# Kernel optimization log

Hardware: AMD Instinct MI355X
Metric: run time of the kernel (lower is better)

The kernel has to match this reference:

```python
import jax, jax.numpy as jnp
import numpy as np

N = 100000      # nodes
E = 1600000     # edges (avg degree 16)
F_IN = 128      # node feature dim
F_OUT = 128     # GCN output dim


def setup_inputs() -> dict:
    key = jax.random.key(0)
    ks = jax.random.split(key, 11)
    s = 0.05  # weight scale to keep activations sane
    return {
        "x": jax.random.normal(ks[0], (N, F_IN), jnp.float32),
        "edge_index": jax.random.randint(ks[1], (2, E), 0, N, jnp.int32),
        "W": jax.random.normal(ks[2], (F_IN, F_OUT), jnp.float32) * s,
        "p": jax.random.normal(ks[3], (F_IN,), jnp.float32),
        "w_ih": jax.random.normal(ks[4], (3 * F_OUT, F_IN), jnp.float32) * s,
        "w_hh": jax.random.normal(ks[5], (3 * F_OUT, F_OUT), jnp.float32) * s,
        "b_ih": jax.random.normal(ks[6], (3 * F_OUT,), jnp.float32) * s,
        "b_hh": jax.random.normal(ks[7], (3 * F_OUT,), jnp.float32) * s,
        "conv_bias": jax.random.normal(ks[8], (F_OUT,), jnp.float32) * s,
        "lin_w": jax.random.normal(ks[9], (1, F_OUT), jnp.float32) * s,
        "lin_b": jax.random.normal(ks[10], (1,), jnp.float32) * s,
    }


def reference(x, edge_index, W, p, w_ih, w_hh, b_ih, b_hh, conv_bias, lin_w, lin_b):
    n_nodes = x.shape[0]
    k, H = W.shape  # k = F_IN rows, H = F_OUT hidden size

    # --- TopK summarize: pick k nodes, gate by tanh(score) -> X_tilde [k, F_IN]
    scores = x @ p / jnp.linalg.norm(p)
    top_vals, top_idx = jax.lax.top_k(scores, k)
    x_tilde = x[top_idx] * jnp.tanh(top_vals)[:, None]

    # --- one GRU step evolving W (hidden state = rows of W)
    gi = x_tilde @ w_ih.T + b_ih   # [k, 3H]
    gh = W @ w_hh.T + b_hh         # [k, 3H]
    r = jax.nn.sigmoid(gi[:, :H] + gh[:, :H])
    z = jax.nn.sigmoid(gi[:, H:2 * H] + gh[:, H:2 * H])
    n = jnp.tanh(gi[:, 2 * H:] + r * gh[:, 2 * H:])
    W_new = (1.0 - z) * n + z * W  # [F_IN, F_OUT]

    # --- GCN conv with fixed W: sym-normalized adjacency with self loops
    row, col = edge_index[0], edge_index[1]
    deg = jax.ops.segment_sum(jnp.ones_like(row, dtype=x.dtype), col,
                              num_segments=n_nodes) + 1.0  # +1 for self loop
    dinv = jax.lax.rsqrt(deg)
    xw = x @ W_new                                   # [N, F_OUT]
    coef = dinv[row] * dinv[col]                     # [E]
    agg = jax.ops.segment_sum(xw[row] * coef[:, None], col, num_segments=n_nodes)
    agg = agg + xw * (dinv * dinv)[:, None] + conv_bias  # self-loop term + bias

    # --- head: ReLU + Linear(F_OUT, 1)
    h = jax.nn.relu(agg)
    return h @ lin_w.T + lin_b  # [N, 1]
```

## Files before the change

kernel.cpp:

```cpp
#include <hip/hip_runtime.h>
#include <math.h>

#define N_NODES 100000
#define N_EDGES 1600000
#define F 128

#define BSH 9
#define NBUCK 196
#define BCAP 10240
#define PB_EDGES 4096

typedef unsigned int u32;
typedef unsigned short u16;
typedef __attribute__((ext_vector_type(8))) short short8;
typedef __attribute__((ext_vector_type(4))) float floatx4;


__device__ __forceinline__ u32 key_of(float s) {
    u32 u = __float_as_uint(s);
    return (u & 0x80000000u) ? ~u : (u | 0x80000000u);
}

__device__ __forceinline__ float wave_reduce(float v) {
    #pragma unroll
    for (int off = 32; off > 0; off >>= 1) v += __shfl_down(v, off, 64);
    return v;
}

__device__ __forceinline__ u16 f2bf(float f) {
    u32 u = __float_as_uint(f);
    u += 0x7fffu + ((u >> 16) & 1u);
    return (u16)(u >> 16);
}

__device__ __forceinline__ float bflo(u32 b) { return __uint_as_float(b << 16); }
__device__ __forceinline__ float bfhi(u32 b) { return __uint_as_float(b & 0xffff0000u); }


__global__ void k_scores(const float* __restrict__ x, const float* __restrict__ p,
                         float* __restrict__ scores, u32* __restrict__ hist16) {
    int node = blockIdx.x * 4 + (threadIdx.x >> 6);
    int lane = threadIdx.x & 63;
    if (node >= N_NODES) return;
    float2 xv = *(const float2*)&x[(size_t)node * F + lane * 2];
    float2 pv = *(const float2*)&p[lane * 2];
    float d = xv.x * pv.x + xv.y * pv.y;
    d = wave_reduce(d);
    if (lane == 0) {
        scores[node] = d;
        atomicAdd(&hist16[key_of(d) >> 16], 1u);
    }
}


__global__ __launch_bounds__(1024) void k_scan16(const u32* __restrict__ hist16,
                                                 u32* __restrict__ state) {
    __shared__ u32 a[1024];
    int t = threadIdx.x;
    const uint4* h4 = (const uint4*)hist16;
    u32 local = 0;
    #pragma unroll
    for (int i = 0; i < 16; i++) {
        uint4 v = h4[t * 16 + i];
        local += v.x + v.y + v.z + v.w;
    }
    a[t] = local;
    __syncthreads();
    for (int off = 1; off < 1024; off <<= 1) {
        u32 add = (t + off < 1024) ? a[t + off] : 0u;
        __syncthreads();
        a[t] += add;
        __syncthreads();
    }
    u32 S_above = (t == 1023) ? 0u : a[t + 1];
    if (S_above < 128u && a[t] >= 128u) {
        u32 cum = S_above;
        for (int v = t * 64 + 63; v >= t * 64; v--) {
            cum += hist16[v];
            if (cum >= 128u) { state[0] = (u32)v; break; }
        }
    }
}

__global__ void k_collect16(const float* __restrict__ scores, u32* __restrict__ state,
                            u32* __restrict__ cand) {
    u32 T = state[0] << 16;
    int i = blockIdx.x * blockDim.x + threadIdx.x;
    if (i < N_NODES) {
        if (key_of(scores[i]) >= T) {
            u32 pos = atomicAdd(&state[2], 1u);
            if (pos < 2048u) cand[pos] = (u32)i;
        }
    }
}

__global__ void k_assemble16(const float* __restrict__ scores, const float* __restrict__ p,
                             const u32* __restrict__ state, const u32* __restrict__ cand,
                             u32* __restrict__ top_idx, float* __restrict__ gate) {
    __shared__ u32 ci[2048];
    __shared__ float csc[2048];
    __shared__ float s_inv;
    int t = threadIdx.x;
    if (t < 64) {
        float2 pv = *(const float2*)&p[t * 2];
        float d = pv.x * pv.x + pv.y * pv.y;
        d = wave_reduce(d);
        if (t == 0) s_inv = rsqrtf(d);
    }
    u32 nc = state[2]; if (nc > 2048u) nc = 2048u;
    for (u32 i = t; i < nc; i += 256) { u32 ix = cand[i]; ci[i] = ix; csc[i] = scores[ix]; }
    __syncthreads();
    for (u32 i = t; i < nc; i += 256) {
        u32 myk = key_of(csc[i]);
        u32 myi = ci[i];
        int rank = 0;
        for (u32 j = 0; j < nc; j++) {
            u32 ok = key_of(csc[j]);
            rank += (int)((ok > myk) || (ok == myk && ci[j] < myi));
        }
        if (rank < 128) {
            top_idx[rank] = myi;
            gate[rank] = tanhf(csc[i] * s_inv);
        }
    }
}


__global__ __launch_bounds__(256) void k_ggemm(const float* __restrict__ x,
                                               const float* __restrict__ W,
                                               const float* __restrict__ w_ih,
                                               const float* __restrict__ w_hh,
                                               const u32* __restrict__ top_idx,
                                               const float* __restrict__ gate,
                                               float* __restrict__ G) {
    __shared__ float As[32][128];
    __shared__ float Bs[64][131];
    int t = threadIdx.x;
    int k0 = blockIdx.x * 32;
    int by = blockIdx.y;
    int j0 = by * 64;
    bool is_gi = (by < 6);
    #pragma unroll
    for (int i = 0; i < 4; i++) {
        int l = t + i * 256;
        int row = l >> 5, c4 = l & 31;
        float4 v;
        if (is_gi) {
            u32 idx = top_idx[k0 + row];
            float gt = gate[k0 + row];
            v = *(const float4*)&x[(size_t)idx * F + c4 * 4];
            v.x *= gt; v.y *= gt; v.z *= gt; v.w *= gt;
        } else {
            v = *(const float4*)&W[(k0 + row) * F + c4 * 4];
        }
        *(float4*)&As[row][c4 * 4] = v;
    }
    const float* mat = is_gi ? w_ih : w_hh;
    int jbase = is_gi ? j0 : (j0 - 384);
    #pragma unroll
    for (int i = 0; i < 8; i++) {
        int l = t + i * 256;
        int row = l >> 5, c4 = l & 31;
        float4 v = *(const float4*)&mat[(jbase + row) * F + c4 * 4];
        Bs[row][c4 * 4 + 0] = v.x; Bs[row][c4 * 4 + 1] = v.y;
        Bs[row][c4 * 4 + 2] = v.z; Bs[row][c4 * 4 + 3] = v.w;
    }
    __syncthreads();
    int ty = t >> 5, tx = t & 31;
    float acc[4][2] = {};
    #pragma unroll 4
    for (int f = 0; f < 128; f++) {
        float b0 = Bs[tx * 2][f], b1 = Bs[tx * 2 + 1][f];
        #pragma unroll
        for (int i = 0; i < 4; i++) {
            float a = As[ty * 4 + i][f];
            acc[i][0] += a * b0;
            acc[i][1] += a * b1;
        }
    }
    #pragma unroll
    for (int i = 0; i < 4; i++) {
        int k = k0 + ty * 4 + i;
        G[(size_t)k * 768 + j0 + tx * 2 + 0] = acc[i][0];
        G[(size_t)k * 768 + j0 + tx * 2 + 1] = acc[i][1];
    }
}


__global__ void k_gate(const float* __restrict__ G, const float* __restrict__ W,
                       const float* __restrict__ b_ih, const float* __restrict__ b_hh,
                       float* __restrict__ Wnew, u16* __restrict__ Bfrag) {
    int idx = blockIdx.x * blockDim.x + threadIdx.x;
    int k = idx >> 7, h = idx & 127;
    const float* gk = &G[(size_t)k * 768];
    float gir = gk[h]       + b_ih[h];
    float giz = gk[128 + h] + b_ih[128 + h];
    float gin = gk[256 + h] + b_ih[256 + h];
    float ghr = gk[384 + h] + b_hh[h];
    float ghz = gk[512 + h] + b_hh[128 + h];
    float ghn = gk[640 + h] + b_hh[256 + h];
    float wv  = W[k * F + h];
    float rg = 1.0f / (1.0f + expf(-(gir + ghr)));
    float z  = 1.0f / (1.0f + expf(-(giz + ghz)));
    float n  = tanhf(gin + rg * ghn);
    float val = (1.0f - z) * n + z * wv;
    Wnew[k * F + h] = val;
    int nb = h >> 4, kc = k >> 5, q = (k >> 3) & 3, m = h & 15, jj = k & 7;
    Bfrag[(((nb * 4 + kc) * 64) + q * 16 + m) * 8 + jj] = f2bf(val);
}


__global__ void k_part(const int* __restrict__ ei, u32* __restrict__ gcur,
                       u32* __restrict__ pairs) {
    __shared__ u32 lh[NBUCK];
    __shared__ u32 lbase[NBUCK];
    int t = threadIdx.x;
    int e0 = blockIdx.x * PB_EDGES;
    int e1 = e0 + PB_EDGES; if (e1 > N_EDGES) e1 = N_EDGES;
    for (int i = t; i < NBUCK; i += 256) lh[i] = 0u;
    __syncthreads();
    for (int e = e0 + t; e < e1; e += 256)
        atomicAdd(&lh[((u32)ei[N_EDGES + e]) >> BSH], 1u);
    __syncthreads();
    for (int b = t; b < NBUCK; b += 256) {
        u32 c = lh[b];
        lbase[b] = c ? atomicAdd(&gcur[b], c) : 0u;
        lh[b] = 0u;
    }
    __syncthreads();
    for (int e = e0 + t; e < e1; e += 256) {
        u32 d = (u32)ei[N_EDGES + e];
        u32 b = d >> BSH;
        u32 pos = lbase[b] + atomicAdd(&lh[b], 1u);
        pairs[(size_t)b * BCAP + pos] = ((d & 511u) << 17) | (u32)ei[e];
    }
}

__global__ __launch_bounds__(256) void k_csr(const u32* __restrict__ pairs,
                                             const u32* __restrict__ gcur,
                                             u32* __restrict__ offs,
                                             float* __restrict__ dinv,
                                             u32* __restrict__ ebuf) {
    __shared__ u32 h[512];
    __shared__ u32 sc[512];
    __shared__ u32 ps[256];
    int b = blockIdx.x, t = threadIdx.x;
    u32 pv = (t < NBUCK) ? gcur[t] : 0u;
    ps[t] = pv;
    __syncthreads();
    for (int off = 1; off < 256; off <<= 1) {
        u32 add = (t >= off) ? ps[t - off] : 0u;
        __syncthreads();
        ps[t] += add;
        __syncthreads();
    }
    u32 base = ps[b] - gcur[b];
    u32 cnt  = gcur[b];
    const u32* seg = pairs + (size_t)b * BCAP;
    u32 lo = (u32)b << BSH;
    for (int i = t; i < 512; i += 256) h[i] = 0u;
    __syncthreads();
    for (u32 i = t; i < cnt; i += 256)
        atomicAdd(&h[seg[i] >> 17], 1u);
    __syncthreads();
    for (int i = t; i < 512; i += 256) sc[i] = h[i];
    __syncthreads();
    for (int off = 1; off < 512; off <<= 1) {
        int i0 = t, i1 = t + 256;
        u32 v0 = (i0 >= off) ? sc[i0 - off] : 0u;
        u32 v1 = (i1 >= off) ? sc[i1 - off] : 0u;
        __syncthreads();
        sc[i0] += v0; sc[i1] += v1;
        __syncthreads();
    }
    int nn = N_NODES - (int)lo; if (nn > 512) nn = 512;
    for (int i = t; i < nn; i += 256) {
        u32 c = h[i];
        offs[lo + i] = base + (sc[i] - c);
        dinv[lo + i] = rsqrtf((float)c + 1.0f);
    }
    for (int i = t; i < 512; i += 256) sc[i] -= h[i];
    __syncthreads();
    for (u32 i = t; i < cnt; i += 256) {
        u32 pr = seg[i];
        u32 pos = base + atomicAdd(&sc[pr >> 17], 1u);
        ebuf[pos] = pr & 0x1ffffu;
    }
    if (b == 0 && t == 0) offs[N_NODES] = N_EDGES;
}


__global__ __launch_bounds__(256) void k_gemm(const float* __restrict__ x,
                                              const u16* __restrict__ Bfrag,
                                              const float* __restrict__ dinv,
                                              u16* __restrict__ yw) {
    __shared__ __align__(16) u16 As[8448];
    int t = threadIdx.x;
    int r0 = blockIdx.x * 64;
    #pragma unroll
    for (int i = 0; i < 8; i++) {
        int l = t + i * 256;
        int row = l >> 5, c4 = l & 31;
        int f0 = c4 * 4;
        float4 v = {0.f, 0.f, 0.f, 0.f};
        if (r0 + row < N_NODES) v = *(const float4*)&x[(size_t)(r0 + row) * F + f0];
        int widx = (((row >> 4) * 4 + (f0 >> 5)) * 64 + ((f0 >> 3) & 3) * 16 + (row & 15)) * 8
                   + (f0 & 7);
        ushort4 s4;
        s4.x = f2bf(v.x); s4.y = f2bf(v.y); s4.z = f2bf(v.z); s4.w = f2bf(v.w);
        *(ushort4*)&As[widx] = s4;
    }
    __syncthreads();

    int wv = t >> 6, lane = t & 63;
    int q = lane >> 4, m = lane & 15;
    floatx4 acc[8] = {};
    #pragma unroll
    for (int kc = 0; kc < 4; kc++) {
        short8 a = *(const short8*)&As[((wv * 4 + kc) * 64 + lane) * 8];
        #pragma unroll
        for (int nb = 0; nb < 8; nb++) {
            short8 bfr = *(const short8*)&Bfrag[((nb * 4 + kc) * 64 + lane) * 8];
            acc[nb] = __builtin_amdgcn_mfma_f32_16x16x32_bf16(a, bfr, acc[nb], 0, 0, 0);
        }
    }
    __syncthreads();

    float d[4];
    #pragma unroll
    for (int reg = 0; reg < 4; reg++) {
        int gr = r0 + wv * 16 + q * 4 + reg;
        d[reg] = (gr < N_NODES) ? dinv[gr] : 0.f;
    }
    #pragma unroll
    for (int nb = 0; nb < 8; nb++) {
        #pragma unroll
        for (int reg = 0; reg < 4; reg++) {
            int row = wv * 16 + q * 4 + reg;
            As[row * 132 + nb * 16 + m] = f2bf(acc[nb][reg] * d[reg]);
        }
    }
    __syncthreads();
    {
        int row = t >> 2, segi = t & 3;
        int gr = r0 + row;
        if (gr < N_NODES) {
            const uint2* src = (const uint2*)&As[row * 132 + segi * 32];
            uint2* dst = (uint2*)&yw[(size_t)gr * F + segi * 32];
            #pragma unroll
            for (int i = 0; i < 8; i++) dst[i] = src[i];
        }
    }
}


#define EDGE_GROUP(J) {                                                      \
    u32 r = ebuf[(J) + q];                                                   \
    uint4 bb = *(const uint4*)&yw32[(size_t)r * 64 + sub * 4];               \
    a0 += bflo(bb.x); a1 += bfhi(bb.x);                                      \
    a2 += bflo(bb.y); a3 += bfhi(bb.y);                                      \
    a4 += bflo(bb.z); a5 += bfhi(bb.z);                                      \
    a6 += bflo(bb.w); a7 += bfhi(bb.w); }

__global__ void k_gather(const u32* __restrict__ yw32, const u32* __restrict__ offs,
                         const u32* __restrict__ ebuf, const float* __restrict__ dinv,
                         const float* __restrict__ conv_bias, const float* __restrict__ lin_w,
                         const float* __restrict__ lin_b, float* __restrict__ out) {
    int c = blockIdx.x * 4 + (threadIdx.x >> 6);
    if (c >= N_NODES) return;
    int lane = threadIdx.x & 63;
    int q = lane >> 4, sub = lane & 15;
    u32 jbeg = offs[c], jend = offs[c + 1];
    float a0 = 0.f, a1 = 0.f, a2 = 0.f, a3 = 0.f;
    float a4 = 0.f, a5 = 0.f, a6 = 0.f, a7 = 0.f;
    u32 j = jbeg;
    for (; j + 16 <= jend; j += 16) {
        EDGE_GROUP(j) EDGE_GROUP(j + 4) EDGE_GROUP(j + 8) EDGE_GROUP(j + 12)
    }
    for (; j + 4 <= jend; j += 4) EDGE_GROUP(j)
    u32 rem = jend - j;
    if (rem) {
        u32 idx = ((u32)q < rem) ? (j + q) : (jend - 1);
        u32 r = ebuf[idx];
        float mk = ((u32)q < rem) ? 1.f : 0.f;
        uint4 bb = *(const uint4*)&yw32[(size_t)r * 64 + sub * 4];
        a0 += mk * bflo(bb.x); a1 += mk * bfhi(bb.x);
        a2 += mk * bflo(bb.y); a3 += mk * bfhi(bb.y);
        a4 += mk * bflo(bb.z); a5 += mk * bfhi(bb.z);
        a6 += mk * bflo(bb.w); a7 += mk * bfhi(bb.w);
    }
    a0 += __shfl_xor(a0, 16, 64); a0 += __shfl_xor(a0, 32, 64);
    a1 += __shfl_xor(a1, 16, 64); a1 += __shfl_xor(a1, 32, 64);
    a2 += __shfl_xor(a2, 16, 64); a2 += __shfl_xor(a2, 32, 64);
    a3 += __shfl_xor(a3, 16, 64); a3 += __shfl_xor(a3, 32, 64);
    a4 += __shfl_xor(a4, 16, 64); a4 += __shfl_xor(a4, 32, 64);
    a5 += __shfl_xor(a5, 16, 64); a5 += __shfl_xor(a5, 32, 64);
    a6 += __shfl_xor(a6, 16, 64); a6 += __shfl_xor(a6, 32, 64);
    a7 += __shfl_xor(a7, 16, 64); a7 += __shfl_xor(a7, 32, 64);
    float dc = dinv[c];
    uint4 sb = *(const uint4*)&yw32[(size_t)c * 64 + sub * 4];
    float4 cb0 = *(const float4*)&conv_bias[sub * 8];
    float4 cb1 = *(const float4*)&conv_bias[sub * 8 + 4];
    float4 lw0 = *(const float4*)&lin_w[sub * 8];
    float4 lw1 = *(const float4*)&lin_w[sub * 8 + 4];
    float h0 = fmaxf(dc * (a0 + bflo(sb.x)) + cb0.x, 0.f);
    float h1 = fmaxf(dc * (a1 + bfhi(sb.x)) + cb0.y, 0.f);
    float h2 = fmaxf(dc * (a2 + bflo(sb.y)) + cb0.z, 0.f);
    float h3 = fmaxf(dc * (a3 + bfhi(sb.y)) + cb0.w, 0.f);
    float h4 = fmaxf(dc * (a4 + bflo(sb.z)) + cb1.x, 0.f);
    float h5 = fmaxf(dc * (a5 + bfhi(sb.z)) + cb1.y, 0.f);
    float h6 = fmaxf(dc * (a6 + bflo(sb.w)) + cb1.z, 0.f);
    float h7 = fmaxf(dc * (a7 + bfhi(sb.w)) + cb1.w, 0.f);
    float part = (h0 * lw0.x + h1 * lw0.y + h2 * lw0.z + h3 * lw0.w)
               + (h4 * lw1.x + h5 * lw1.y + h6 * lw1.z + h7 * lw1.w);
    part = (q == 0) ? part : 0.f;
    part = wave_reduce(part);
    if (lane == 0) out[c] = part + lin_b[0];
}


extern "C" void kernel_launch(void* const* d_in, const int* in_sizes, int n_in,
                              void* d_out, int out_size, void* d_ws, size_t ws_size,
                              hipStream_t stream) {
    const float* x         = (const float*)d_in[0];
    const int*   ei        = (const int*)  d_in[1];
    const float* W         = (const float*)d_in[2];
    const float* p         = (const float*)d_in[3];
    const float* w_ih      = (const float*)d_in[4];
    const float* w_hh      = (const float*)d_in[5];
    const float* b_ih      = (const float*)d_in[6];
    const float* b_hh      = (const float*)d_in[7];
    const float* conv_bias = (const float*)d_in[8];
    const float* lin_w     = (const float*)d_in[9];
    const float* lin_b     = (const float*)d_in[10];
    float* out = (float*)d_out;

    u32*   w  = (u32*)d_ws;
    float* wf = (float*)d_ws;

    const size_t SCORES_W = 0;
    const size_t DINV_W   = 100096;
    const size_t OFFS_W   = 200192;
    const size_t HIST16_W = 300288;
    const size_t STATE_W  = 365824;
    const size_t GCUR_W   = 365832;
    const size_t CAND_W   = 366080;
    const size_t TOPI_W   = 368128;
    const size_t GATE_W   = 368256;
    const size_t WNEW_W   = 368384;
    const size_t BFRAG_W  = 384768;
    const size_t PAIRS_W  = 392960;
    const size_t EBUF_W   = 2400000;
    const size_t YW_W     = 4000000;

    float* scores  = wf + SCORES_W;
    float* dinv    = wf + DINV_W;
    u32*   offs    = w  + OFFS_W;
    u32*   hist16  = w  + HIST16_W;
    u32*   state   = w  + STATE_W;
    u32*   gcur    = w  + GCUR_W;
    u32*   cand    = w  + CAND_W;
    u32*   top_idx = w  + TOPI_W;
    float* gate    = wf + GATE_W;
    float* Wnew    = wf + WNEW_W;
    u16*   Bfrag   = (u16*)(w + BFRAG_W);
    u32*   pairs   = w  + PAIRS_W;
    float* G       = wf + PAIRS_W;
    u32*   ebuf    = w  + EBUF_W;
    u16*   yw      = (u16*)(w + YW_W);
    u32*   yw32    = w + YW_W;

    hipMemsetAsync(hist16, 0, (65536 + 8 + NBUCK) * sizeof(u32), stream);

    k_scores<<<25000, 256, 0, stream>>>(x, p, scores, hist16);
    k_scan16<<<1, 1024, 0, stream>>>(hist16, state);
    k_collect16<<<392, 256, 0, stream>>>(scores, state, cand);
    k_assemble16<<<1, 256, 0, stream>>>(scores, p, state, cand, top_idx, gate);

    k_ggemm<<<dim3(4, 12), 256, 0, stream>>>(x, W, w_ih, w_hh, top_idx, gate, G);
    k_gate<<<64, 256, 0, stream>>>(G, W, b_ih, b_hh, Wnew, Bfrag);

    k_part<<<(N_EDGES + PB_EDGES - 1) / PB_EDGES, 256, 0, stream>>>(ei, gcur, pairs);
    k_csr<<<NBUCK, 256, 0, stream>>>(pairs, gcur, offs, dinv, ebuf);

    k_gemm<<<1563, 256, 0, stream>>>(x, Bfrag, dinv, yw);

    k_gather<<<25000, 256, 0, stream>>>(yw32, offs, ebuf, dinv, conv_bias, lin_w,
                                        lin_b, out);
}
```

Baseline: 325.9 us.

## Fuse scoring with edge partitioning, collect with CSR build; prepack bf16 x

Scoring and edge bucketing now run in one launch split by block range, and candidate collection and CSR construction share a second launch. This removes two launches and lets independent work run side by side. When the workspace is large enough, the scoring pass also writes a bf16 copy of x, so the projection GEMM loads half the bytes; in exchange the scoring pass writes that extra buffer. The gather kernel switches to packed f32 adds, non-temporal index loads and a shorter final reduction.

```diff
diff --git a/kernel.cpp b/kernel.cpp
--- a/kernel.cpp
+++ b/kernel.cpp
@@ -9,11 +9,15 @@
 #define NBUCK 196
 #define BCAP 10240
 #define PB_EDGES 4096
+#define NB_SCORES 25000
+#define NB_PART 391
+#define NB_COLLECT 392
 
 typedef unsigned int u32;
 typedef unsigned short u16;
 typedef __attribute__((ext_vector_type(8))) short short8;
 typedef __attribute__((ext_vector_type(4))) float floatx4;
+typedef __attribute__((ext_vector_type(2))) float f32x2;
 
 
 __device__ __forceinline__ u32 key_of(float s) {
@@ -36,19 +40,56 @@
 __device__ __forceinline__ float bflo(u32 b) { return __uint_as_float(b << 16); }
 __device__ __forceinline__ float bfhi(u32 b) { return __uint_as_float(b & 0xffff0000u); }
 
-
-__global__ void k_scores(const float* __restrict__ x, const float* __restrict__ p,
-                         float* __restrict__ scores, u32* __restrict__ hist16) {
-    int node = blockIdx.x * 4 + (threadIdx.x >> 6);
-    int lane = threadIdx.x & 63;
-    if (node >= N_NODES) return;
-    float2 xv = *(const float2*)&x[(size_t)node * F + lane * 2];
-    float2 pv = *(const float2*)&p[lane * 2];
-    float d = xv.x * pv.x + xv.y * pv.y;
-    d = wave_reduce(d);
-    if (lane == 0) {
-        scores[node] = d;
-        atomicAdd(&hist16[key_of(d) >> 16], 1u);
+__device__ __forceinline__ void pk_acc(f32x2& acc, u32 u) {
+    f32x2 v; v.x = bflo(u); v.y = bfhi(u);
+    asm("v_pk_add_f32 %0, %1, %0" : "+v"(acc) : "v"(v));
+}
+__device__ __forceinline__ void pk_add2(f32x2& a, f32x2 b) {
+    asm("v_pk_add_f32 %0, %1, %0" : "+v"(a) : "v"(b));
+}
+
+
+__global__ void k_front(const float* __restrict__ x, const float* __restrict__ p,
+                        const int* __restrict__ ei, float* __restrict__ scores,
+                        u32* __restrict__ hist16, u32* __restrict__ gcur,
+                        u32* __restrict__ pairs, u32* __restrict__ xb) {
+    if (blockIdx.x < NB_SCORES) {
+        int node = blockIdx.x * 4 + (threadIdx.x >> 6);
+        int lane = threadIdx.x & 63;
+        if (node >= N_NODES) return;
+        float2 xv = *(const float2*)&x[(size_t)node * F + lane * 2];
+        float2 pv = *(const float2*)&p[lane * 2];
+        if (xb)
+            xb[(size_t)node * 64 + lane] = (u32)f2bf(xv.x) | ((u32)f2bf(xv.y) << 16);
+        float d = xv.x * pv.x + xv.y * pv.y;
+        d = wave_reduce(d);
+        if (lane == 0) {
+            scores[node] = d;
+            atomicAdd(&hist16[key_of(d) >> 16], 1u);
+        }
+    } else {
+        __shared__ u32 lh[NBUCK];
+        __shared__ u32 lbase[NBUCK];
+        int t = threadIdx.x;
+        int e0 = (blockIdx.x - NB_SCORES) * PB_EDGES;
+        int e1 = e0 + PB_EDGES; if (e1 > N_EDGES) e1 = N_EDGES;
+        for (int i = t; i < NBUCK; i += 256) lh[i] = 0u;
+        __syncthreads();
+        for (int e = e0 + t; e < e1; e += 256)
+            atomicAdd(&lh[((u32)ei[N_EDGES + e]) >> BSH], 1u);
+        __syncthreads();
+        for (int b = t; b < NBUCK; b += 256) {
+            u32 c = lh[b];
+            lbase[b] = c ? atomicAdd(&gcur[b], c) : 0u;
+            lh[b] = 0u;
+        }
+        __syncthreads();
+        for (int e = e0 + t; e < e1; e += 256) {
+            u32 d = (u32)ei[N_EDGES + e];
+            u32 b = d >> BSH;
+            u32 pos = lbase[b] + atomicAdd(&lh[b], 1u);
+            pairs[(size_t)b * BCAP + pos] = ((d & 511u) << 17) | (u32)ei[e];
+        }
     }
 }
 
@@ -82,15 +123,71 @@
     }
 }
 
-__global__ void k_collect16(const float* __restrict__ scores, u32* __restrict__ state,
-                            u32* __restrict__ cand) {
-    u32 T = state[0] << 16;
-    int i = blockIdx.x * blockDim.x + threadIdx.x;
-    if (i < N_NODES) {
-        if (key_of(scores[i]) >= T) {
-            u32 pos = atomicAdd(&state[2], 1u);
-            if (pos < 2048u) cand[pos] = (u32)i;
-        }
+
+__global__ __launch_bounds__(256) void k_mid(const float* __restrict__ scores,
+                                             u32* __restrict__ state,
+                                             u32* __restrict__ cand,
+                                             const u32* __restrict__ pairs,
+                                             const u32* __restrict__ gcur,
+                                             u32* __restrict__ offs,
+                                             float* __restrict__ dinv,
+                                             u32* __restrict__ ebuf) {
+    if (blockIdx.x < NB_COLLECT) {
+        u32 T = state[0] << 16;
+        int i = blockIdx.x * 256 + threadIdx.x;
+        if (i < N_NODES) {
+            if (key_of(scores[i]) >= T) {
+                u32 pos = atomicAdd(&state[2], 1u);
+                if (pos < 2048u) cand[pos] = (u32)i;
+            }
+        }
+    } else {
+        __shared__ u32 h[512];
+        __shared__ u32 sc[512];
+        __shared__ u32 ps[256];
+        int b = blockIdx.x - NB_COLLECT, t = threadIdx.x;
+        u32 pv = (t < NBUCK) ? gcur[t] : 0u;
+        ps[t] = pv;
+        __syncthreads();
+        for (int off = 1; off < 256; off <<= 1) {
+            u32 add = (t >= off) ? ps[t - off] : 0u;
+            __syncthreads();
+            ps[t] += add;
+            __syncthreads();
+        }
+        u32 base = ps[b] - gcur[b];
+        u32 cnt  = gcur[b];
+        const u32* seg = pairs + (size_t)b * BCAP;
+        u32 lo = (u32)b << BSH;
+        for (int i = t; i < 512; i += 256) h[i] = 0u;
+        __syncthreads();
+        for (u32 i = t; i < cnt; i += 256)
+            atomicAdd(&h[seg[i] >> 17], 1u);
+        __syncthreads();
+        for (int i = t; i < 512; i += 256) sc[i] = h[i];
+        __syncthreads();
+        for (int off = 1; off < 512; off <<= 1) {
+            int i0 = t, i1 = t + 256;
+            u32 v0 = (i0 >= off) ? sc[i0 - off] : 0u;
+            u32 v1 = (i1 >= off) ? sc[i1 - off] : 0u;
+            __syncthreads();
+            sc[i0] += v0; sc[i1] += v1;
+            __syncthreads();
+        }
+        int nn = N_NODES - (int)lo; if (nn > 512) nn = 512;
+        for (int i = t; i < nn; i += 256) {
+            u32 c = h[i];
+            offs[lo + i] = base + (sc[i] - c);
+            dinv[lo + i] = rsqrtf((float)c + 1.0f);
+        }
+        for (int i = t; i < 512; i += 256) sc[i] -= h[i];
+        __syncthreads();
+        for (u32 i = t; i < cnt; i += 256) {
+            u32 pr = seg[i];
+            u32 pos = base + atomicAdd(&sc[pr >> 17], 1u);
+            ebuf[pos] = pr & 0x1ffffu;
+        }
+        if (b == 0 && t == 0) offs[N_NODES] = N_EDGES;
     }
 }
 
@@ -210,85 +307,49 @@
 }
 
 
-__global__ void k_part(const int* __restrict__ ei, u32* __restrict__ gcur,
-                       u32* __restrict__ pairs) {
-    __shared__ u32 lh[NBUCK];
-    __shared__ u32 lbase[NBUCK];
-    int t = threadIdx.x;
-    int e0 = blockIdx.x * PB_EDGES;
-    int e1 = e0 + PB_EDGES; if (e1 > N_EDGES) e1 = N_EDGES;
-    for (int i = t; i < NBUCK; i += 256) lh[i] = 0u;
-    __syncthreads();
-    for (int e = e0 + t; e < e1; e += 256)
-        atomicAdd(&lh[((u32)ei[N_EDGES + e]) >> BSH], 1u);
-    __syncthreads();
-    for (int b = t; b < NBUCK; b += 256) {
-        u32 c = lh[b];
-        lbase[b] = c ? atomicAdd(&gcur[b], c) : 0u;
-        lh[b] = 0u;
-    }
-    __syncthreads();
-    for (int e = e0 + t; e < e1; e += 256) {
-        u32 d = (u32)ei[N_EDGES + e];
-        u32 b = d >> BSH;
-        u32 pos = lbase[b] + atomicAdd(&lh[b], 1u);
-        pairs[(size_t)b * BCAP + pos] = ((d & 511u) << 17) | (u32)ei[e];
-    }
-}
-
-__global__ __launch_bounds__(256) void k_csr(const u32* __restrict__ pairs,
-                                             const u32* __restrict__ gcur,
-                                             u32* __restrict__ offs,
-                                             float* __restrict__ dinv,
-                                             u32* __restrict__ ebuf) {
-    __shared__ u32 h[512];
-    __shared__ u32 sc[512];
-    __shared__ u32 ps[256];
-    int b = blockIdx.x, t = threadIdx.x;
-    u32 pv = (t < NBUCK) ? gcur[t] : 0u;
-    ps[t] = pv;
-    __syncthreads();
-    for (int off = 1; off < 256; off <<= 1) {
-        u32 add = (t >= off) ? ps[t - off] : 0u;
-        __syncthreads();
-        ps[t] += add;
-        __syncthreads();
-    }
-    u32 base = ps[b] - gcur[b];
-    u32 cnt  = gcur[b];
-    const u32* seg = pairs + (size_t)b * BCAP;
-    u32 lo = (u32)b << BSH;
-    for (int i = t; i < 512; i += 256) h[i] = 0u;
-    __syncthreads();
-    for (u32 i = t; i < cnt; i += 256)
-        atomicAdd(&h[seg[i] >> 17], 1u);
-    __syncthreads();
-    for (int i = t; i < 512; i += 256) sc[i] = h[i];
-    __syncthreads();
-    for (int off = 1; off < 512; off <<= 1) {
-        int i0 = t, i1 = t + 256;
-        u32 v0 = (i0 >= off) ? sc[i0 - off] : 0u;
-        u32 v1 = (i1 >= off) ? sc[i1 - off] : 0u;
-        __syncthreads();
-        sc[i0] += v0; sc[i1] += v1;
-        __syncthreads();
-    }
-    int nn = N_NODES - (int)lo; if (nn > 512) nn = 512;
-    for (int i = t; i < nn; i += 256) {
-        u32 c = h[i];
-        offs[lo + i] = base + (sc[i] - c);
-        dinv[lo + i] = rsqrtf((float)c + 1.0f);
-    }
-    for (int i = t; i < 512; i += 256) sc[i] -= h[i];
-    __syncthreads();
-    for (u32 i = t; i < cnt; i += 256) {
-        u32 pr = seg[i];
-        u32 pos = base + atomicAdd(&sc[pr >> 17], 1u);
-        ebuf[pos] = pr & 0x1ffffu;
-    }
-    if (b == 0 && t == 0) offs[N_NODES] = N_EDGES;
-}
-
+__device__ __forceinline__ void gemm_core(u16* As, const u16* __restrict__ Bfrag,
+                                          const float* __restrict__ dinv,
+                                          u16* __restrict__ yw, int r0, int t) {
+    int wv = t >> 6, lane = t & 63;
+    int q = lane >> 4, m = lane & 15;
+    floatx4 acc[8] = {};
+    #pragma unroll
+    for (int kc = 0; kc < 4; kc++) {
+        short8 a = *(const short8*)&As[((wv * 4 + kc) * 64 + lane) * 8];
+        #pragma unroll
+        for (int nb = 0; nb < 8; nb++) {
+            short8 bfr = *(const short8*)&Bfrag[((nb * 4 + kc) * 64 + lane) * 8];
+            acc[nb] = __builtin_amdgcn_mfma_f32_16x16x32_bf16(a, bfr, acc[nb], 0, 0, 0);
+        }
+    }
+    __syncthreads();
+
+    float d[4];
+    #pragma unroll
+    for (int reg = 0; reg < 4; reg++) {
+        int gr = r0 + wv * 16 + q * 4 + reg;
+        d[reg] = (gr < N_NODES) ? dinv[gr] : 0.f;
+    }
+    #pragma unroll
+    for (int nb = 0; nb < 8; nb++) {
+        #pragma unroll
+        for (int reg = 0; reg < 4; reg++) {
+            int row = wv * 16 + q * 4 + reg;
+            As[row * 132 + nb * 16 + m] = f2bf(acc[nb][reg] * d[reg]);
+        }
+    }
+    __syncthreads();
+    {
+        int row = t >> 2, segi = t & 3;
+        int gr = r0 + row;
+        if (gr < N_NODES) {
+            const uint2* src = (const uint2*)&As[row * 132 + segi * 32];
+            uint2* dst = (uint2*)&yw[(size_t)gr * F + segi * 32];
+            #pragma unroll
+            for (int i = 0; i < 8; i++) dst[i] = src[i];
+        }
+    }
+}
 
 __global__ __launch_bounds__(256) void k_gemm(const float* __restrict__ x,
                                               const u16* __restrict__ Bfrag,
@@ -311,56 +372,45 @@
         *(ushort4*)&As[widx] = s4;
     }
     __syncthreads();
-
-    int wv = t >> 6, lane = t & 63;
-    int q = lane >> 4, m = lane & 15;
-    floatx4 acc[8] = {};
-    #pragma unroll
-    for (int kc = 0; kc < 4; kc++) {
-        short8 a = *(const short8*)&As[((wv * 4 + kc) * 64 + lane) * 8];
-        #pragma unroll
-        for (int nb = 0; nb < 8; nb++) {
-            short8 bfr = *(const short8*)&Bfrag[((nb * 4 + kc) * 64 + lane) * 8];
-            acc[nb] = __builtin_amdgcn_mfma_f32_16x16x32_bf16(a, bfr, acc[nb], 0, 0, 0);
-        }
-    }
-    __syncthreads();
-
-    float d[4];
-    #pragma unroll
-    for (int reg = 0; reg < 4; reg++) {
-        int gr = r0 + wv * 16 + q * 4 + reg;
-        d[reg] = (gr < N_NODES) ? dinv[gr] : 0.f;
-    }
-    #pragma unroll
-    for (int nb = 0; nb < 8; nb++) {
-        #pragma unroll
-        for (int reg = 0; reg < 4; reg++) {
-            int row = wv * 16 + q * 4 + reg;
-            As[row * 132 + nb * 16 + m] = f2bf(acc[nb][reg] * d[reg]);
-        }
-    }
-    __syncthreads();
-    {
-        int row = t >> 2, segi = t & 3;
-        int gr = r0 + row;
-        if (gr < N_NODES) {
-            const uint2* src = (const uint2*)&As[row * 132 + segi * 32];
-            uint2* dst = (uint2*)&yw[(size_t)gr * F + segi * 32];
-            #pragma unroll
-            for (int i = 0; i < 8; i++) dst[i] = src[i];
-        }
-    }
+    gemm_core(As, Bfrag, dinv, yw, r0, t);
+}
+
+__global__ __launch_bounds__(256) void k_gemm_xb(const u32* __restrict__ xb,
+                                                 const u16* __restrict__ Bfrag,
+                                                 const float* __restrict__ dinv,
+                                                 u16* __restrict__ yw) {
+    __shared__ __align__(16) u16 As[8448];
+    int t = threadIdx.x;
+    int r0 = blockIdx.x * 64;
+    #pragma unroll
+    for (int i = 0; i < 4; i++) {
+        int wdx = t + i * 256;
+        int lane = wdx & 63, chunk = wdx >> 6;
+        int kc = chunk & 3, rowhi = chunk >> 2;
+        int q = lane >> 4, m = lane & 15;
+        int row = rowhi * 16 + m;
+        uint4 v = {0u, 0u, 0u, 0u};
+        if (r0 + row < N_NODES)
+            v = *(const uint4*)&xb[(size_t)(r0 + row) * 64 + kc * 16 + q * 4];
+        *(uint4*)&As[wdx * 8] = v;
+    }
+    __syncthreads();
+    gemm_core(As, Bfrag, dinv, yw, r0, t);
 }
 
 
 #define EDGE_GROUP(J) {                                                      \
-    u32 r = ebuf[(J) + q];                                                   \
+    u32 r = __builtin_nontemporal_load(&ebuf[(J) + q]);                      \
     uint4 bb = *(const uint4*)&yw32[(size_t)r * 64 + sub * 4];               \
-    a0 += bflo(bb.x); a1 += bfhi(bb.x);                                      \
-    a2 += bflo(bb.y); a3 += bfhi(bb.y);                                      \
-    a4 += bflo(bb.z); a5 += bfhi(bb.z);                                      \
-    a6 += bflo(bb.w); a7 += bfhi(bb.w); }
+    pk_acc(a01, bb.x); pk_acc(a23, bb.y);                                    \
+    pk_acc(a45, bb.z); pk_acc(a67, bb.w); }
+
+#define BFLY(A) {                                                            \
+    f32x2 tb;                                                                \
+    tb.x = __shfl_xor(A.x, 16, 64); tb.y = __shfl_xor(A.y, 16, 64);          \
+    pk_add2(A, tb);                                                          \
+    tb.x = __shfl_xor(A.x, 32, 64); tb.y = __shfl_xor(A.y, 32, 64);          \
+    pk_add2(A, tb); }
 
 __global__ void k_gather(const u32* __restrict__ yw32, const u32* __restrict__ offs,
                          const u32* __restrict__ ebuf, const float* __restrict__ dinv,
@@ -371,8 +421,7 @@
     int lane = threadIdx.x & 63;
     int q = lane >> 4, sub = lane & 15;
     u32 jbeg = offs[c], jend = offs[c + 1];
-    float a0 = 0.f, a1 = 0.f, a2 = 0.f, a3 = 0.f;
-    float a4 = 0.f, a5 = 0.f, a6 = 0.f, a7 = 0.f;
+    f32x2 a01 = {0.f, 0.f}, a23 = {0.f, 0.f}, a45 = {0.f, 0.f}, a67 = {0.f, 0.f};
     u32 j = jbeg;
     for (; j + 16 <= jend; j += 16) {
         EDGE_GROUP(j) EDGE_GROUP(j + 4) EDGE_GROUP(j + 8) EDGE_GROUP(j + 12)
@@ -380,41 +429,33 @@
     for (; j + 4 <= jend; j += 4) EDGE_GROUP(j)
     u32 rem = jend - j;
     if (rem) {
-        u32 idx = ((u32)q < rem) ? (j + q) : (jend - 1);
-        u32 r = ebuf[idx];
-        float mk = ((u32)q < rem) ? 1.f : 0.f;
+        u32 idx = ((u32)q < rem) ? (j + q) : j;
+        u32 r = __builtin_nontemporal_load(&ebuf[idx]);
         uint4 bb = *(const uint4*)&yw32[(size_t)r * 64 + sub * 4];
-        a0 += mk * bflo(bb.x); a1 += mk * bfhi(bb.x);
-        a2 += mk * bflo(bb.y); a3 += mk * bfhi(bb.y);
-        a4 += mk * bflo(bb.z); a5 += mk * bfhi(bb.z);
-        a6 += mk * bflo(bb.w); a7 += mk * bfhi(bb.w);
-    }
-    a0 += __shfl_xor(a0, 16, 64); a0 += __shfl_xor(a0, 32, 64);
-    a1 += __shfl_xor(a1, 16, 64); a1 += __shfl_xor(a1, 32, 64);
-    a2 += __shfl_xor(a2, 16, 64); a2 += __shfl_xor(a2, 32, 64);
-    a3 += __shfl_xor(a3, 16, 64); a3 += __shfl_xor(a3, 32, 64);
-    a4 += __shfl_xor(a4, 16, 64); a4 += __shfl_xor(a4, 32, 64);
-    a5 += __shfl_xor(a5, 16, 64); a5 += __shfl_xor(a5, 32, 64);
-    a6 += __shfl_xor(a6, 16, 64); a6 += __shfl_xor(a6, 32, 64);
-    a7 += __shfl_xor(a7, 16, 64); a7 += __shfl_xor(a7, 32, 64);
+        if ((u32)q < rem) {
+            pk_acc(a01, bb.x); pk_acc(a23, bb.y);
+            pk_acc(a45, bb.z); pk_acc(a67, bb.w);
+        }
+    }
+    BFLY(a01) BFLY(a23) BFLY(a45) BFLY(a67)
     float dc = dinv[c];
     uint4 sb = *(const uint4*)&yw32[(size_t)c * 64 + sub * 4];
     float4 cb0 = *(const float4*)&conv_bias[sub * 8];
     float4 cb1 = *(const float4*)&conv_bias[sub * 8 + 4];
     float4 lw0 = *(const float4*)&lin_w[sub * 8];
     float4 lw1 = *(const float4*)&lin_w[sub * 8 + 4];
-    float h0 = fmaxf(dc * (a0 + bflo(sb.x)) + cb0.x, 0.f);
-    float h1 = fmaxf(dc * (a1 + bfhi(sb.x)) + cb0.y, 0.f);
-    float h2 = fmaxf(dc * (a2 + bflo(sb.y)) + cb0.z, 0.f);
-    float h3 = fmaxf(dc * (a3 + bfhi(sb.y)) + cb0.w, 0.f);
-    float h4 = fmaxf(dc * (a4 + bflo(sb.z)) + cb1.x, 0.f);
-    float h5 = fmaxf(dc * (a5 + bfhi(sb.z)) + cb1.y, 0.f);
-    float h6 = fmaxf(dc * (a6 + bflo(sb.w)) + cb1.z, 0.f);
-    float h7 = fmaxf(dc * (a7 + bfhi(sb.w)) + cb1.w, 0.f);
+    float h0 = fmaxf(dc * (a01.x + bflo(sb.x)) + cb0.x, 0.f);
+    float h1 = fmaxf(dc * (a01.y + bfhi(sb.x)) + cb0.y, 0.f);
+    float h2 = fmaxf(dc * (a23.x + bflo(sb.y)) + cb0.z, 0.f);
+    float h3 = fmaxf(dc * (a23.y + bfhi(sb.y)) + cb0.w, 0.f);
+    float h4 = fmaxf(dc * (a45.x + bflo(sb.z)) + cb1.x, 0.f);
+    float h5 = fmaxf(dc * (a45.y + bfhi(sb.z)) + cb1.y, 0.f);
+    float h6 = fmaxf(dc * (a67.x + bflo(sb.w)) + cb1.z, 0.f);
+    float h7 = fmaxf(dc * (a67.y + bfhi(sb.w)) + cb1.w, 0.f);
     float part = (h0 * lw0.x + h1 * lw0.y + h2 * lw0.z + h3 * lw0.w)
                + (h4 * lw1.x + h5 * lw1.y + h6 * lw1.z + h7 * lw1.w);
-    part = (q == 0) ? part : 0.f;
-    part = wave_reduce(part);
+    #pragma unroll
+    for (int off = 8; off > 0; off >>= 1) part += __shfl_down(part, off, 64);
     if (lane == 0) out[c] = part + lin_b[0];
 }
 
@@ -452,6 +493,7 @@
     const size_t PAIRS_W  = 392960;
     const size_t EBUF_W   = 2400000;
     const size_t YW_W     = 4000000;
+    const size_t XB_W     = 10400000;
 
     float* scores  = wf + SCORES_W;
     float* dinv    = wf + DINV_W;
@@ -470,20 +512,23 @@
     u16*   yw      = (u16*)(w + YW_W);
     u32*   yw32    = w + YW_W;
 
+    bool   use_xb  = ws_size >= (XB_W + 6400000) * sizeof(u32);
+    u32*   xb      = use_xb ? (w + XB_W) : (u32*)0;
+
     hipMemsetAsync(hist16, 0, (65536 + 8 + NBUCK) * sizeof(u32), stream);
 
-    k_scores<<<25000, 256, 0, stream>>>(x, p, scores, hist16);
+    k_front<<<NB_SCORES + NB_PART, 256, 0, stream>>>(x, p, ei, scores, hist16,
+                                                     gcur, pairs, xb);
     k_scan16<<<1, 1024, 0, stream>>>(hist16, state);
-    k_collect16<<<392, 256, 0, stream>>>(scores, state, cand);
+    k_mid<<<NB_COLLECT + NBUCK, 256, 0, stream>>>(scores, state, cand, pairs, gcur,
+                                                  offs, dinv, ebuf);
     k_assemble16<<<1, 256, 0, stream>>>(scores, p, state, cand, top_idx, gate);
 
     k_ggemm<<<dim3(4, 12), 256, 0, stream>>>(x, W, w_ih, w_hh, top_idx, gate, G);
     k_gate<<<64, 256, 0, stream>>>(G, W, b_ih, b_hh, Wnew, Bfrag);
 
-    k_part<<<(N_EDGES + PB_EDGES - 1) / PB_EDGES, 256, 0, stream>>>(ei, gcur, pairs);
-    k_csr<<<NBUCK, 256, 0, stream>>>(pairs, gcur, offs, dinv, ebuf);
-
-    k_gemm<<<1563, 256, 0, stream>>>(x, Bfrag, dinv, yw);
+    if (use_xb) k_gemm_xb<<<1563, 256, 0, stream>>>(xb, Bfrag, dinv, yw);
+    else        k_gemm   <<<1563, 256, 0, stream>>>(x,  Bfrag, dinv, yw);
 
     k_gather<<<25000, 256, 0, stream>>>(yw32, offs, ebuf, dinv, conv_bias, lin_w,
                                         lin_b, out);
```

Measured after the change: 321.5 us. No clear change (-1.3%).
